# Kernel optimization log

Hardware: AMD Instinct MI355X
Metric: run time of the kernel (lower is better)

Reference implementation:

```python
import jax, jax.numpy as jnp
import numpy as np

TAU_MIN = 0.001
XPBD_ITERS = 4
XPBD_COMPLIANCE = 0.0
XPBD_MAX_CORR = 0.15

B, N, D, E = 4, 50000, 256, 800000


def setup_inputs() -> dict:
    key = jax.random.key(0)
    ks = jax.random.split(key, 7)
    keypoints = jax.random.normal(ks[0], (B, N, 3), dtype=jnp.float32)
    timesteps = jax.random.uniform(ks[1], (B,), dtype=jnp.float32)
    hand_tokens = jax.random.normal(ks[2], (B, N, D), dtype=jnp.float32)
    head_w = jax.random.normal(ks[3], (D, 3), dtype=jnp.float32) * 0.02
    head_b = jnp.zeros((3,), dtype=jnp.float32)
    edge_index = jax.random.randint(ks[4], (2, E), 0, N, dtype=jnp.int32)
    rest_lengths = jax.random.uniform(ks[5], (E,), dtype=jnp.float32) + 0.1
    return {
        "keypoints": keypoints,
        "timesteps": timesteps,
        "hand_tokens": hand_tokens,
        "head_w": head_w,
        "head_b": head_b,
        "edge_index": edge_index,
        "rest_lengths": rest_lengths,
    }


def _xpbd_project(x, src, dst, rest_lengths):
    # x: (B, N, 3); src/dst: (E,); rest_lengths: (E,)
    L0 = rest_lengths[None, :, None]          # (1, E, 1)
    w_i = 1.0                                  # inv_mass is None -> unit inverse masses
    w_j = 1.0
    alpha = XPBD_COMPLIANCE / (float(XPBD_ITERS) + 1e-08)
    denom = w_i + w_j + alpha + 1e-09
    for _ in range(XPBD_ITERS):
        diff = x[:, src] - x[:, dst]           # (B, E, 3) edge gather
        dist = jnp.linalg.norm(diff, axis=-1, keepdims=True)  # (B, E, 1)
        C = dist - L0
        n = diff / (dist + 1e-09)
        d_lambda = -C / denom
        correction = jnp.clip(d_lambda * n, -XPBD_MAX_CORR, XPBD_MAX_CORR)
        delta = (jnp.zeros_like(x)
                 .at[:, src].add(w_i * correction)
                 .at[:, dst].add(-w_j * correction))  # scatter-add back to nodes
        x = x + delta
    return x


def reference(keypoints, timesteps, hand_tokens, head_w, head_b, edge_index, rest_lengths):
    # tau = clamp(1 - t, min=tau_min), broadcast to (B, 1, 1)
    tau = jnp.maximum(1.0 - timesteps, TAU_MIN)[:, None, None]
    v_raw = hand_tokens @ head_w + head_b      # (B, N, 3) velocity head
    x_pred = keypoints + tau * v_raw
    src = edge_index[0]
    dst = edge_index[1]
    x_corrected = _xpbd_project(x_pred, src, dst, rest_lengths)
    v_eff = (x_corrected - keypoints) / tau
    return v_eff
```

## Files before the change

### kernel.cpp

```cpp
#include <hip/hip_runtime.h>

#define BB 4
#define NN 50000
#define DD 256
#define EE 800000
#define TAU_MIN_F 0.001f
#define MAX_CORR_F 0.15f

#define CAP 80
#define NPART 8
#define PNODES (NN / NPART)
#define PS_CE 2048
#define PS_NCHUNK ((EE + PS_CE - 1) / PS_CE)
#define NBUCKET (NPART * PS_NCHUNK)
#define XPB 2048
#define S1_GRID (NBUCKET + XPB)
#define NWAVE (XPB * 4)

__device__ __forceinline__ float wsum64(float x) {
    x += __int_as_float(__builtin_amdgcn_update_dpp(0, __float_as_int(x), 0x111, 0xf, 0xf, true));
    x += __int_as_float(__builtin_amdgcn_update_dpp(0, __float_as_int(x), 0x112, 0xf, 0xf, true));
    x += __int_as_float(__builtin_amdgcn_update_dpp(0, __float_as_int(x), 0x114, 0xf, 0xf, true));
    x += __int_as_float(__builtin_amdgcn_update_dpp(0, __float_as_int(x), 0x118, 0xf, 0xf, true));
    x += __int_as_float(__builtin_amdgcn_update_dpp(0, __float_as_int(x), 0x142, 0xf, 0xf, true));
    x += __int_as_float(__builtin_amdgcn_update_dpp(0, __float_as_int(x), 0x143, 0xf, 0xf, true));
    return x;
}

__global__ __launch_bounds__(256) void stage1_kernel(
    const float* __restrict__ kp, const float* __restrict__ ts,
    const float* __restrict__ ht, const float* __restrict__ hw,
    const float* __restrict__ hb, float4* __restrict__ x,
    const int* __restrict__ ei, const float* __restrict__ L0,
    int* __restrict__ counts, int2* __restrict__ adj)
{
    if ((int)blockIdx.x < NBUCKET) {
        const int part  = (int)blockIdx.x & 7;
        const int chunk = (int)blockIdx.x >> 3;
        const int lo   = part * PNODES;
        const int hi   = lo + PNODES;
        const int base = chunk * PS_CE;
        const int eEnd = min(base + PS_CE, EE);
        for (int e = base + (int)threadIdx.x; e < eEnd; e += 256) {
            const int s = ei[e];
            const int d = ei[EE + e];
            const int r = __float_as_int(L0[e]);
            const bool hs = (s >= lo) & (s < hi);
            const bool hd = (d >= lo) & (d < hi);
            int ps = CAP, pd = CAP;
            if (hs) ps = atomicAdd(&counts[s], 1);
            if (hd) pd = atomicAdd(&counts[d], 1);
            if (hs && ps < CAP) adj[s * CAP + ps] = make_int2(d << 2, r);
            if (hd && pd < CAP) adj[d * CAP + pd] = make_int2(s << 2, r);
        }
        return;
    }

    const int lane = threadIdx.x & 63;
    const int wave = (((int)blockIdx.x - NBUCKET) * 256 + (int)threadIdx.x) >> 6;
    const int d0   = lane * 4;

    float W[4][3];
#pragma unroll
    for (int j = 0; j < 4; ++j)
#pragma unroll
        for (int k = 0; k < 3; ++k)
            W[j][k] = hw[(d0 + j) * 3 + k];
    const float b0 = hb[0], b1 = hb[1], b2 = hb[2];

    int i = wave;
    for (; i + NWAVE < BB * NN; i += 2 * NWAVE) {
        const int iA = i, iB = i + NWAVE;
        const int rowA = (iA & 3) * NN + (iA >> 2);
        const int rowB = (iB & 3) * NN + (iB >> 2);
        const float4 hA = *(const float4*)(ht + (size_t)rowA * DD + d0);
        const float4 hB = *(const float4*)(ht + (size_t)rowB * DD + d0);
        float aA0 = hA.x * W[0][0] + hA.y * W[1][0] + hA.z * W[2][0] + hA.w * W[3][0];
        float aA1 = hA.x * W[0][1] + hA.y * W[1][1] + hA.z * W[2][1] + hA.w * W[3][1];
        float aA2 = hA.x * W[0][2] + hA.y * W[1][2] + hA.z * W[2][2] + hA.w * W[3][2];
        float aB0 = hB.x * W[0][0] + hB.y * W[1][0] + hB.z * W[2][0] + hB.w * W[3][0];
        float aB1 = hB.x * W[0][1] + hB.y * W[1][1] + hB.z * W[2][1] + hB.w * W[3][1];
        float aB2 = hB.x * W[0][2] + hB.y * W[1][2] + hB.z * W[2][2] + hB.w * W[3][2];
        aA0 = wsum64(aA0);  aB0 = wsum64(aB0);
        aA1 = wsum64(aA1);  aB1 = wsum64(aB1);
        aA2 = wsum64(aA2);  aB2 = wsum64(aB2);
        if (lane == 63) {
            {
                const float tau = fmaxf(1.0f - ts[iA & 3], TAU_MIN_F);
                float4 v;
                v.x = kp[rowA * 3 + 0] + tau * (aA0 + b0);
                v.y = kp[rowA * 3 + 1] + tau * (aA1 + b1);
                v.z = kp[rowA * 3 + 2] + tau * (aA2 + b2);
                v.w = 0.0f;
                x[iA] = v;
            }
            {
                const float tau = fmaxf(1.0f - ts[iB & 3], TAU_MIN_F);
                float4 v;
                v.x = kp[rowB * 3 + 0] + tau * (aB0 + b0);
                v.y = kp[rowB * 3 + 1] + tau * (aB1 + b1);
                v.z = kp[rowB * 3 + 2] + tau * (aB2 + b2);
                v.w = 0.0f;
                x[iB] = v;
            }
        }
    }
    if (i < BB * NN) {
        const int row = (i & 3) * NN + (i >> 2);
        const float4 h = *(const float4*)(ht + (size_t)row * DD + d0);
        float a0 = h.x * W[0][0] + h.y * W[1][0] + h.z * W[2][0] + h.w * W[3][0];
        float a1 = h.x * W[0][1] + h.y * W[1][1] + h.z * W[2][1] + h.w * W[3][1];
        float a2 = h.x * W[0][2] + h.y * W[1][2] + h.z * W[2][2] + h.w * W[3][2];
        a0 = wsum64(a0);  a1 = wsum64(a1);  a2 = wsum64(a2);
        if (lane == 63) {
            const float tau = fmaxf(1.0f - ts[i & 3], TAU_MIN_F);
            float4 v;
            v.x = kp[row * 3 + 0] + tau * (a0 + b0);
            v.y = kp[row * 3 + 1] + tau * (a1 + b1);
            v.z = kp[row * 3 + 2] + tau * (a2 + b2);
            v.w = 0.0f;
            x[i] = v;
        }
    }
}

__global__ __launch_bounds__(256) void gather_kernel(
    const float4* __restrict__ xin, float4* __restrict__ xout,
    const int* __restrict__ counts, const int2* __restrict__ adj,
    const float* __restrict__ kp, const float* __restrict__ ts,
    float* __restrict__ out, int final_iter)
{
    const int tid  = blockIdx.x * 256 + threadIdx.x;
    const int b    = tid & 3;
    const int sub  = (tid >> 2) & 7;
    const int node = tid >> 5;

    const float4 xc = xin[(node << 2) + b];
    float a0 = 0.0f, a1 = 0.0f, a2 = 0.0f;

    const int beg = node * CAP;
    const int cnt = min(counts[node], CAP);
    const int seg = ((cnt + 15) >> 4) << 1;
    int k        = beg + sub * seg;
    const int ke = min(k + seg, beg + cnt);

    for (; k + 1 < ke; k += 2) {
        const int4 e = *(const int4*)(&adj[k]);
        const float4 n0 = xin[e.x + b];
        const float4 n1 = xin[e.z + b];
        {
            const float dx = xc.x - n0.x, dy = xc.y - n0.y, dz = xc.z - n0.z;
            const float dist = sqrtf(dx * dx + dy * dy + dz * dz);
            const float s = (__int_as_float(e.y) - dist) * 0.5f / (dist + 1e-9f);
            a0 += fminf(fmaxf(s * dx, -MAX_CORR_F), MAX_CORR_F);
            a1 += fminf(fmaxf(s * dy, -MAX_CORR_F), MAX_CORR_F);
            a2 += fminf(fmaxf(s * dz, -MAX_CORR_F), MAX_CORR_F);
        }
        {
            const float dx = xc.x - n1.x, dy = xc.y - n1.y, dz = xc.z - n1.z;
            const float dist = sqrtf(dx * dx + dy * dy + dz * dz);
            const float s = (__int_as_float(e.w) - dist) * 0.5f / (dist + 1e-9f);
            a0 += fminf(fmaxf(s * dx, -MAX_CORR_F), MAX_CORR_F);
            a1 += fminf(fmaxf(s * dy, -MAX_CORR_F), MAX_CORR_F);
            a2 += fminf(fmaxf(s * dz, -MAX_CORR_F), MAX_CORR_F);
        }
    }
    if (k < ke) {
        const int2 e0 = adj[k];
        const float4 n0 = xin[e0.x + b];
        const float dx = xc.x - n0.x, dy = xc.y - n0.y, dz = xc.z - n0.z;
        const float dist = sqrtf(dx * dx + dy * dy + dz * dz);
        const float s = (__int_as_float(e0.y) - dist) * 0.5f / (dist + 1e-9f);
        a0 += fminf(fmaxf(s * dx, -MAX_CORR_F), MAX_CORR_F);
        a1 += fminf(fmaxf(s * dy, -MAX_CORR_F), MAX_CORR_F);
        a2 += fminf(fmaxf(s * dz, -MAX_CORR_F), MAX_CORR_F);
    }

    a0 += __shfl_xor(a0, 4);  a0 += __shfl_xor(a0, 8);  a0 += __shfl_xor(a0, 16);
    a1 += __shfl_xor(a1, 4);  a1 += __shfl_xor(a1, 8);  a1 += __shfl_xor(a1, 16);
    a2 += __shfl_xor(a2, 4);  a2 += __shfl_xor(a2, 8);  a2 += __shfl_xor(a2, 16);

    if (sub == 0) {
        if (!final_iter) {
            float4 v; v.x = xc.x + a0; v.y = xc.y + a1; v.z = xc.z + a2; v.w = 0.0f;
            xout[(node << 2) + b] = v;
        } else {
            const int row = b * NN + node;
            const float tau = fmaxf(1.0f - ts[b], TAU_MIN_F);
            const float it  = 1.0f / tau;
            out[row * 3 + 0] = (xc.x + a0 - kp[row * 3 + 0]) * it;
            out[row * 3 + 1] = (xc.y + a1 - kp[row * 3 + 1]) * it;
            out[row * 3 + 2] = (xc.z + a2 - kp[row * 3 + 2]) * it;
        }
    }
}

extern "C" void kernel_launch(void* const* d_in, const int* in_sizes, int n_in,
                              void* d_out, int out_size, void* d_ws, size_t ws_size,
                              hipStream_t stream)
{
    const float* kp = (const float*)d_in[0];
    const float* ts = (const float*)d_in[1];
    const float* ht = (const float*)d_in[2];
    const float* hw = (const float*)d_in[3];
    const float* hb = (const float*)d_in[4];
    const int*   ei = (const int*)d_in[5];
    const float* L0 = (const float*)d_in[6];
    float* out = (float*)d_out;

    char* w = (char*)d_ws;
    int2*   adj    = (int2*)w;                 w += (size_t)NN * CAP * sizeof(int2);
    float4* xA     = (float4*)w;               w += (size_t)BB * NN * sizeof(float4);
    float4* xB     = (float4*)w;               w += (size_t)BB * NN * sizeof(float4);
    int*    counts = (int*)w;

    hipMemsetAsync(counts, 0, (size_t)NN * sizeof(int), stream);

    stage1_kernel<<<S1_GRID, 256, 0, stream>>>(kp, ts, ht, hw, hb, xA,
                                               ei, L0, counts, adj);

    const int gatherBlocks = (32 * NN) / 256;
    gather_kernel<<<gatherBlocks, 256, 0, stream>>>(xA, xB, counts, adj, kp, ts, out, 0);
    gather_kernel<<<gatherBlocks, 256, 0, stream>>>(xB, xA, counts, adj, kp, ts, out, 0);
    gather_kernel<<<gatherBlocks, 256, 0, stream>>>(xA, xB, counts, adj, kp, ts, out, 0);
    gather_kernel<<<gatherBlocks, 256, 0, stream>>>(xB, xA, counts, adj, kp, ts, out, 1);
}
```

Before: 443.4 us.

## Split fused stage1 into separate xpred and bucket kernels with nontemporal streaming loads

The combined stage-one kernel, which ran the velocity-head projection and the adjacency bucketing in one grid, is split into two kernels launched back to back. The streaming reads of hand tokens, edge indices and rest lengths, and the final output stores, become nontemporal so they do not pollute the cache needed by the atomics and later gathers. The split removes the overlap the fused grid allowed between the bandwidth-bound matvec and the atomic-heavy bucketing, and adds one kernel launch.

```diff
diff --git a/kernel.cpp b/kernel.cpp
--- a/kernel.cpp
+++ b/kernel.cpp
@@ -14,8 +14,10 @@
 #define PS_NCHUNK ((EE + PS_CE - 1) / PS_CE)
 #define NBUCKET (NPART * PS_NCHUNK)
 #define XPB 2048
-#define S1_GRID (NBUCKET + XPB)
 #define NWAVE (XPB * 4)
+
+typedef float  f4 __attribute__((ext_vector_type(4)));
+typedef int    i2 __attribute__((ext_vector_type(2)));
 
 __device__ __forceinline__ float wsum64(float x) {
     x += __int_as_float(__builtin_amdgcn_update_dpp(0, __float_as_int(x), 0x111, 0xf, 0xf, true));
@@ -27,37 +29,13 @@
     return x;
 }
 
-__global__ __launch_bounds__(256) void stage1_kernel(
+__global__ __launch_bounds__(256) void xpred_kernel(
     const float* __restrict__ kp, const float* __restrict__ ts,
     const float* __restrict__ ht, const float* __restrict__ hw,
-    const float* __restrict__ hb, float4* __restrict__ x,
-    const int* __restrict__ ei, const float* __restrict__ L0,
-    int* __restrict__ counts, int2* __restrict__ adj)
-{
-    if ((int)blockIdx.x < NBUCKET) {
-        const int part  = (int)blockIdx.x & 7;
-        const int chunk = (int)blockIdx.x >> 3;
-        const int lo   = part * PNODES;
-        const int hi   = lo + PNODES;
-        const int base = chunk * PS_CE;
-        const int eEnd = min(base + PS_CE, EE);
-        for (int e = base + (int)threadIdx.x; e < eEnd; e += 256) {
-            const int s = ei[e];
-            const int d = ei[EE + e];
-            const int r = __float_as_int(L0[e]);
-            const bool hs = (s >= lo) & (s < hi);
-            const bool hd = (d >= lo) & (d < hi);
-            int ps = CAP, pd = CAP;
-            if (hs) ps = atomicAdd(&counts[s], 1);
-            if (hd) pd = atomicAdd(&counts[d], 1);
-            if (hs && ps < CAP) adj[s * CAP + ps] = make_int2(d << 2, r);
-            if (hd && pd < CAP) adj[d * CAP + pd] = make_int2(s << 2, r);
-        }
-        return;
-    }
-
+    const float* __restrict__ hb, float4* __restrict__ x)
+{
     const int lane = threadIdx.x & 63;
-    const int wave = (((int)blockIdx.x - NBUCKET) * 256 + (int)threadIdx.x) >> 6;
+    const int wave = ((int)blockIdx.x * 256 + (int)threadIdx.x) >> 6;
     const int d0   = lane * 4;
 
     float W[4][3];
@@ -73,8 +51,8 @@
         const int iA = i, iB = i + NWAVE;
         const int rowA = (iA & 3) * NN + (iA >> 2);
         const int rowB = (iB & 3) * NN + (iB >> 2);
-        const float4 hA = *(const float4*)(ht + (size_t)rowA * DD + d0);
-        const float4 hB = *(const float4*)(ht + (size_t)rowB * DD + d0);
+        const f4 hA = __builtin_nontemporal_load((const f4*)(ht + (size_t)rowA * DD + d0));
+        const f4 hB = __builtin_nontemporal_load((const f4*)(ht + (size_t)rowB * DD + d0));
         float aA0 = hA.x * W[0][0] + hA.y * W[1][0] + hA.z * W[2][0] + hA.w * W[3][0];
         float aA1 = hA.x * W[0][1] + hA.y * W[1][1] + hA.z * W[2][1] + hA.w * W[3][1];
         float aA2 = hA.x * W[0][2] + hA.y * W[1][2] + hA.z * W[2][2] + hA.w * W[3][2];
@@ -107,7 +85,7 @@
     }
     if (i < BB * NN) {
         const int row = (i & 3) * NN + (i >> 2);
-        const float4 h = *(const float4*)(ht + (size_t)row * DD + d0);
+        const f4 h = __builtin_nontemporal_load((const f4*)(ht + (size_t)row * DD + d0));
         float a0 = h.x * W[0][0] + h.y * W[1][0] + h.z * W[2][0] + h.w * W[3][0];
         float a1 = h.x * W[0][1] + h.y * W[1][1] + h.z * W[2][1] + h.w * W[3][1];
         float a2 = h.x * W[0][2] + h.y * W[1][2] + h.z * W[2][2] + h.w * W[3][2];
@@ -124,6 +102,30 @@
     }
 }
 
+__global__ __launch_bounds__(256) void pbucket_kernel(
+    const int* __restrict__ ei, const float* __restrict__ L0,
+    int* __restrict__ counts, int2* __restrict__ adj)
+{
+    const int part  = (int)blockIdx.x & 7;
+    const int chunk = (int)blockIdx.x >> 3;
+    const int lo   = part * PNODES;
+    const int hi   = lo + PNODES;
+    const int base = chunk * PS_CE;
+    const int eEnd = min(base + PS_CE, EE);
+    for (int e = base + (int)threadIdx.x; e < eEnd; e += 256) {
+        const int s = __builtin_nontemporal_load(ei + e);
+        const int d = __builtin_nontemporal_load(ei + EE + e);
+        const int r = __float_as_int(__builtin_nontemporal_load(L0 + e));
+        const bool hs = (s >= lo) & (s < hi);
+        const bool hd = (d >= lo) & (d < hi);
+        int ps = CAP, pd = CAP;
+        if (hs) ps = atomicAdd(&counts[s], 1);
+        if (hd) pd = atomicAdd(&counts[d], 1);
+        if (hs && ps < CAP) adj[s * CAP + ps] = make_int2(d << 2, r);
+        if (hd && pd < CAP) adj[d * CAP + pd] = make_int2(s << 2, r);
+    }
+}
+
 __global__ __launch_bounds__(256) void gather_kernel(
     const float4* __restrict__ xin, float4* __restrict__ xout,
     const int* __restrict__ counts, const int2* __restrict__ adj,
@@ -187,10 +189,10 @@
         } else {
             const int row = b * NN + node;
             const float tau = fmaxf(1.0f - ts[b], TAU_MIN_F);
-            const float it  = 1.0f / tau;
-            out[row * 3 + 0] = (xc.x + a0 - kp[row * 3 + 0]) * it;
-            out[row * 3 + 1] = (xc.y + a1 - kp[row * 3 + 1]) * it;
-            out[row * 3 + 2] = (xc.z + a2 - kp[row * 3 + 2]) * it;
+            const float itau = 1.0f / tau;
+            __builtin_nontemporal_store((xc.x + a0 - kp[row * 3 + 0]) * itau, out + row * 3 + 0);
+            __builtin_nontemporal_store((xc.y + a1 - kp[row * 3 + 1]) * itau, out + row * 3 + 1);
+            __builtin_nontemporal_store((xc.z + a2 - kp[row * 3 + 2]) * itau, out + row * 3 + 2);
         }
     }
 }
@@ -216,8 +218,8 @@
 
     hipMemsetAsync(counts, 0, (size_t)NN * sizeof(int), stream);
 
-    stage1_kernel<<<S1_GRID, 256, 0, stream>>>(kp, ts, ht, hw, hb, xA,
-                                               ei, L0, counts, adj);
+    xpred_kernel<<<XPB, 256, 0, stream>>>(kp, ts, ht, hw, hb, xA);
+    pbucket_kernel<<<NBUCKET, 256, 0, stream>>>(ei, L0, counts, adj);
 
     const int gatherBlocks = (32 * NN) / 256;
     gather_kernel<<<gatherBlocks, 256, 0, stream>>>(xA, xB, counts, adj, kp, ts, out, 0);
```

Measured after the change: 448.5 us. About the same (+1.1%).
